# Kernel tuning notes

Hardware: AMD Instinct MI355X
Metric: run time of the kernel (lower is better)

The kernel has to match this reference:

```python
import jax, jax.numpy as jnp
import numpy as np
from jax import lax

K_KNN = 20           # DGCNN default neighborhood size
SLOPE = 0.2          # LeakyReLU negative slope


def _leaky(x):
    return jnp.where(x >= 0, x, SLOPE * x)


def _knn(x, k):
    # x: [B, N, C] -> idx [B, N, k] of nearest neighbors (incl. self) in feature space
    xx = jnp.sum(x * x, axis=-1)                       # [B, N]
    d = xx[:, :, None] + xx[:, None, :] - 2.0 * jnp.einsum('bnc,bmc->bnm', x, x)
    return lax.top_k(-d, k)[1]                          # [B, N, k]


def _edge_conv(x, idx, w, b):
    # x: [B, N, C]; idx: [B, N, k]; w: [O, 2C]; b: [O]
    neigh = jax.vmap(lambda xt, i: xt[i])(x, idx)       # [B, N, k, C]
    center = jnp.broadcast_to(x[:, :, None, :], neigh.shape)
    feat = jnp.concatenate([neigh - center, center], axis=-1)  # [B, N, k, 2C]
    h = _leaky(jnp.einsum('bnkc,oc->bnko', feat, w) + b)
    return jnp.max(h, axis=2)                           # [B, N, O]


def setup_inputs() -> dict:
    key = jax.random.key(0)
    ks = jax.random.split(key, 20)
    B, N, J, KR = 4, 4096, 24, 4
    layers = [64, 128, 256]

    def w_init(k, o, i):
        return jax.random.normal(k, (o, i), jnp.float32) / np.sqrt(i)

    inp = {
        'V': jax.random.normal(ks[0], (B, N, 3), jnp.float32),
        'W': jax.random.uniform(ks[1], (B, J, N), jnp.float32),
        'skeletonOneRingIdx': jax.random.randint(ks[2], (B, J, KR), 0, J),
    }
    # geoNet edge-conv params (input channels per layer: 3, 64, 128 -> 2C inputs)
    inp['g1_w'] = w_init(ks[3], 64, 6);    inp['g1_b'] = jnp.zeros((64,), jnp.float32)
    inp['g2_w'] = w_init(ks[4], 128, 128); inp['g2_b'] = jnp.zeros((128,), jnp.float32)
    inp['g3_w'] = w_init(ks[5], 256, 256); inp['g3_b'] = jnp.zeros((256,), jnp.float32)
    # skeleton edge-conv params (inputs: 451 -> 902, 256 -> 512, 128 -> 256)
    inp['s1_w'] = w_init(ks[6], 256, 902); inp['s1_b'] = jnp.zeros((256,), jnp.float32)
    inp['s2_w'] = w_init(ks[7], 128, 512); inp['s2_b'] = jnp.zeros((128,), jnp.float32)
    inp['s3_w'] = w_init(ks[8], 64, 256);  inp['s3_b'] = jnp.zeros((64,), jnp.float32)
    # jointMLP 1x1 convs: 448 -> 512 -> 256 -> 3
    inp['m1_w'] = w_init(ks[9], 512, 448);  inp['m1_b'] = jnp.zeros((512,), jnp.float32)
    inp['m2_w'] = w_init(ks[10], 256, 512); inp['m2_b'] = jnp.zeros((256,), jnp.float32)
    inp['m3_w'] = w_init(ks[11], 3, 256);   inp['m3_b'] = jnp.zeros((3,), jnp.float32)
    return inp


def reference(V, W, skeletonOneRingIdx,
              g1_w, g1_b, g2_w, g2_b, g3_w, g3_b,
              s1_w, s1_b, s2_w, s2_b, s3_w, s3_b,
              m1_w, m1_b, m2_w, m2_b, m3_w, m3_b):
    # ---- geoNet: DGCNN with dynamic kNN, output cat([xyz, l1, l2, l3]) -> [B, N, 451]
    outs = [V]
    h = V
    for w, b in ((g1_w, g1_b), (g2_w, g2_b), (g3_w, g3_b)):
        idx = _knn(h, K_KNN)
        h = _edge_conv(h, idx, w, b)
        outs.append(h)
    feat = jnp.concatenate(outs, axis=-1)                # [B, N, 451]

    # ---- weighted pooling onto skeleton joints
    pooled = jnp.einsum('bjn,bnc->bjc', W, feat)
    pooled = pooled / (jnp.sum(W, axis=-1, keepdims=True) + 1e-5)  # [B, J, 451]

    # ---- skeleton edge convs with fixed one-ring idx
    v1 = _edge_conv(pooled, skeletonOneRingIdx, s1_w, s1_b)  # [B, J, 256]
    v2 = _edge_conv(v1, skeletonOneRingIdx, s2_w, s2_b)      # [B, J, 128]
    v3 = _edge_conv(v2, skeletonOneRingIdx, s3_w, s3_b)      # [B, J, 64]

    joints = jnp.concatenate([v1, v2, v3], axis=-1)          # [B, J, 448]
    h = _leaky(jnp.einsum('bjc,oc->bjo', joints, m1_w) + m1_b)
    h = _leaky(jnp.einsum('bjc,oc->bjo', h, m2_w) + m2_b)
    out = jnp.einsum('bjc,oc->bjo', h, m3_w) + m3_b          # [B, J, 3]
    return out
```

## Files before the change

### kernel.cpp

```cpp
#include <hip/hip_runtime.h>
#include <hip/hip_bf16.h>
#include <float.h>

#define B_   4
#define N_   4096
#define J_   24
#define KR_  4
#define KNN_ 20
#define SLOPE 0.2f
#define SLABN 64
#define NSLAB (N_ / SLABN)
#define NTILE 32
#define SCAP 768
#define KSLACK 8u

typedef __attribute__((ext_vector_type(8))) short bf16x8;
typedef __attribute__((ext_vector_type(4))) float f32x4;

__global__ void k_norm(const float* __restrict__ h, float* __restrict__ xx, int C) {
    int i = blockIdx.x * blockDim.x + threadIdx.x;
    if (i >= B_ * N_) return;
    const float* hp = h + (size_t)i * C;
    float s = 0.f;
    for (int c = 0; c < C; ++c) { float v = hp[c]; s += v * v; }
    xx[i] = s;
}

__device__ __forceinline__ unsigned mapf(float f) {
    unsigned u = __float_as_uint(f);
    return (u & 0x80000000u) ? ~u : (u | 0x80000000u);
}
__device__ __forceinline__ unsigned key16(float f) {
    return mapf(f) >> 16;
}

__global__ void k_split(const float* __restrict__ h, unsigned short* __restrict__ hi,
                        unsigned short* __restrict__ lo, int total4) {
    int i = blockIdx.x * 256 + threadIdx.x;
    if (i >= total4) return;
    float4 v = ((const float4*)h)[i];
    ushort4 h4, l4;
    {
        unsigned u = __float_as_uint(v.x); h4.x = (unsigned short)(u >> 16);
        float r = v.x - __uint_as_float(u & 0xffff0000u); l4.x = (unsigned short)(__float_as_uint(r) >> 16);
    }
    {
        unsigned u = __float_as_uint(v.y); h4.y = (unsigned short)(u >> 16);
        float r = v.y - __uint_as_float(u & 0xffff0000u); l4.y = (unsigned short)(__float_as_uint(r) >> 16);
    }
    {
        unsigned u = __float_as_uint(v.z); h4.z = (unsigned short)(u >> 16);
        float r = v.z - __uint_as_float(u & 0xffff0000u); l4.z = (unsigned short)(__float_as_uint(r) >> 16);
    }
    {
        unsigned u = __float_as_uint(v.w); h4.w = (unsigned short)(u >> 16);
        float r = v.w - __uint_as_float(u & 0xffff0000u); l4.w = (unsigned short)(__float_as_uint(r) >> 16);
    }
    ((ushort4*)hi)[i] = h4;
    ((ushort4*)lo)[i] = l4;
}

__global__ __launch_bounds__(256) void k_dist(const unsigned short* __restrict__ Hi,
                                              const unsigned short* __restrict__ Lo,
                                              int C,
                                              const float* __restrict__ xxall,
                                              unsigned short* __restrict__ Dall, int b0) {
    __shared__ unsigned short tile[128][136];
    int b = b0 + blockIdx.y;
    const unsigned short* XH = Hi + (size_t)b * N_ * C;
    const unsigned short* XL = Lo + (size_t)b * N_ * C;
    const float* xxb = xxall + (size_t)b * N_;
    unsigned short* D = Dall + (size_t)blockIdx.y * N_ * N_;

    int t = blockIdx.x;
    int ti = 0;
    while (t >= NTILE - ti) { t -= NTILE - ti; ++ti; }
    int tj = ti + t;
    int row0 = ti * 128, col0 = tj * 128;
    int tid  = threadIdx.x;
    int wv   = tid >> 6, lane = tid & 63;
    int wr   = wv >> 1,  wc   = wv & 1;
    int rbase = row0 + wr * 64;
    int cbase = col0 + wc * 64;
    int lp    = lane & 15;
    int kgrp  = lane >> 4;

    f32x4 acc[4][4];
#pragma unroll
    for (int i = 0; i < 4; ++i)
#pragma unroll
        for (int j = 0; j < 4; ++j) acc[i][j] = (f32x4){0.f, 0.f, 0.f, 0.f};

    for (int ks = 0; ks < C; ks += 32) {
        int kb = ks + kgrp * 8;
        bf16x8 ah[4], al[4];
#pragma unroll
        for (int fi = 0; fi < 4; ++fi) {
            size_t ro = (size_t)(rbase + fi * 16 + lp) * C + kb;
            ah[fi] = *(const bf16x8*)(XH + ro);
            al[fi] = *(const bf16x8*)(XL + ro);
        }
#pragma unroll
        for (int fj = 0; fj < 4; ++fj) {
            size_t co = (size_t)(cbase + fj * 16 + lp) * C + kb;
            bf16x8 bh = *(const bf16x8*)(XH + co);
            bf16x8 bl = *(const bf16x8*)(XL + co);
#pragma unroll
            for (int fi = 0; fi < 4; ++fi) {
                acc[fi][fj] = __builtin_amdgcn_mfma_f32_16x16x32_bf16(ah[fi], bh, acc[fi][fj], 0, 0, 0);
                acc[fi][fj] = __builtin_amdgcn_mfma_f32_16x16x32_bf16(ah[fi], bl, acc[fi][fj], 0, 0, 0);
                acc[fi][fj] = __builtin_amdgcn_mfma_f32_16x16x32_bf16(al[fi], bh, acc[fi][fj], 0, 0, 0);
            }
        }
    }

    float xxrv = xxb[rbase + lane];
    float xxcv = xxb[cbase + lane];
    int rsub = (lane >> 4) * 4;
#pragma unroll
    for (int fi = 0; fi < 4; ++fi) {
#pragma unroll
        for (int fj = 0; fj < 4; ++fj) {
            float xc = __shfl(xxcv, fj * 16 + lp, 64);
#pragma unroll
            for (int r = 0; r < 4; ++r) {
                float xr = __shfl(xxrv, fi * 16 + rsub + r, 64);
                float d = xr + xc - 2.f * acc[fi][fj][r];
                tile[wr * 64 + fi * 16 + rsub + r][wc * 64 + fj * 16 + lp] =
                    (unsigned short)key16(d);
            }
        }
    }
    __syncthreads();

    {
        int r0   = tid >> 4;
        int cseg = (tid & 15) * 8;
#pragma unroll
        for (int q = 0; q < 8; ++q) {
            int row = r0 + q * 16;
            *(uint4*)(D + (size_t)(row0 + row) * N_ + col0 + cseg) =
                *(const uint4*)&tile[row][cseg];
        }
    }
    if (ti == tj) return;
    {
        int c0g = tid >> 4;
        int g   = tid & 15;
#pragma unroll
        for (int cq = 0; cq < 8; ++cq) {
            int c = c0g + cq * 16;
            unsigned short s[8];
#pragma unroll
            for (int q = 0; q < 8; ++q) s[q] = tile[g * 8 + q][c];
            *(uint4*)(D + (size_t)(col0 + c) * N_ + row0 + g * 8) = *(const uint4*)s;
        }
    }
}

__device__ __forceinline__ unsigned radixsel_wave(unsigned val, int r, int nbits) {
    unsigned long long cand = ~0ull;
    unsigned prefix = 0;
    for (int bit = nbits - 1; bit >= 0; --bit) {
        unsigned long long z = cand & __ballot(!((val >> bit) & 1u));
        int cz = __popcll(z);
        if (cz >= r) cand = z;
        else { r -= cz; cand &= ~z; prefix |= 1u << bit; }
    }
    return prefix;
}

__device__ __forceinline__ bool top20_round(unsigned long long key, bool active) {
    unsigned hi = (unsigned)(key >> 32);
    unsigned lo = (unsigned)key;
    unsigned long long amask = __ballot(active);
    int navail = __popcll(amask);
    if (navail <= KNN_) return active;
    int r = KNN_;
    unsigned long long cand = amask;
    unsigned prefix = 0;
    for (int bit = 31; bit >= 0; --bit) {
        unsigned long long z = cand & __ballot(!((hi >> bit) & 1u));
        int cz = __popcll(z);
        if (cz >= r) cand = z;
        else { r -= cz; cand &= ~z; prefix |= 1u << bit; }
    }
    unsigned long long c2 = __ballot(active && hi == prefix);
    unsigned p2 = 0;
    for (int bit = 11; bit >= 0; --bit) {
        unsigned long long z = c2 & __ballot(!((lo >> bit) & 1u));
        int cz = __popcll(z);
        if (cz >= r) c2 = z;
        else { r -= cz; c2 &= ~z; p2 |= 1u << bit; }
    }
    return active && (hi < prefix || (hi == prefix && lo <= p2));
}

__device__ __forceinline__ void final_top20(const unsigned long long* skey, int S,
                                            unsigned long long* wbuf,
                                            int lane, int* idxout, int obase) {
    unsigned long long key = (lane < S) ? skey[lane] : ~0ull;
    bool active = (lane < S) && (lane < 64);
    int consumed = (S < 64) ? S : 64;
    int nw = 0;
    for (;;) {
        bool win = top20_round(key, active);
        unsigned long long wb = __ballot(win);
        nw = __popcll(wb);
        int pos = __popcll(wb & ((1ull << lane) - 1ull));
        if (win) wbuf[pos] = key;
        if (consumed >= S) break;
        int src = consumed + lane - nw;
        key = (lane < nw) ? wbuf[lane] : ((src < S) ? skey[src] : ~0ull);
        active = (lane < nw) || (src >= consumed && src < S);
        consumed += 64 - nw;
    }
    if (lane < nw) {
        unsigned long long mine = wbuf[lane];
        int rank = 0;
        for (int i = 0; i < nw; ++i) rank += (wbuf[i] < mine);
        idxout[obase + rank] = (int)(unsigned)mine;
    }
}

__global__ __launch_bounds__(256) void k_sel(const unsigned short* __restrict__ Dall,
                                             const float* __restrict__ Xall, int C,
                                             const float* __restrict__ xxall,
                                             int* __restrict__ knnIdx, int b0) {
    __shared__ unsigned sidx[SCAP];
    __shared__ unsigned long long skey[SCAP];
    __shared__ unsigned long long wbuf[24];
    __shared__ float qf[128];
    __shared__ unsigned stau[4];
    __shared__ int scnt;
    int b = b0 + blockIdx.y;
    const unsigned short* Db = Dall + (size_t)blockIdx.y * N_ * N_;
    const float* Xb  = Xall + (size_t)b * N_ * C;
    const float* xxb = xxall + (size_t)b * N_;
    int* idxout = knnIdx + (size_t)b * N_ * KNN_;
    int ql   = blockIdx.x;
    int tid  = threadIdx.x;
    int wv   = tid >> 6;
    int lane = tid & 63;
    int gbase = wv * 1024 + lane * 16;
    if (tid == 0) scnt = 0;
    for (int c = tid; c < C; c += 256) qf[c] = Xb[(size_t)ql * C + c];

    const uint4* kp = (const uint4*)(Db + (size_t)ql * N_ + gbase);
    uint4 pa = kp[0], pb = kp[1];
    unsigned kv[16];
    kv[0] = pa.x & 0xffffu;  kv[1] = pa.x >> 16;
    kv[2] = pa.y & 0xffffu;  kv[3] = pa.y >> 16;
    kv[4] = pa.z & 0xffffu;  kv[5] = pa.z >> 16;
    kv[6] = pa.w & 0xffffu;  kv[7] = pa.w >> 16;
    kv[8] = pb.x & 0xffffu;  kv[9] = pb.x >> 16;
    kv[10] = pb.y & 0xffffu; kv[11] = pb.y >> 16;
    kv[12] = pb.z & 0xffffu; kv[13] = pb.z >> 16;
    kv[14] = pb.w & 0xffffu; kv[15] = pb.w >> 16;

    unsigned mn = kv[0];
#pragma unroll
    for (int t = 1; t < 16; ++t) mn = (kv[t] < mn) ? kv[t] : mn;
    unsigned Bw = radixsel_wave(mn, KNN_, 16);
    if (lane == 0) stau[wv] = Bw;
    __syncthreads();
    unsigned tau = stau[0];
    tau = (stau[1] < tau) ? stau[1] : tau;
    tau = (stau[2] < tau) ? stau[2] : tau;
    tau = (stau[3] < tau) ? stau[3] : tau;
    tau += KSLACK;
    if (tau > 0xffffu) tau = 0xffffu;

#pragma unroll
    for (int t = 0; t < 16; ++t) {
        if (kv[t] <= tau) {
            int p = atomicAdd(&scnt, 1);
            if (p < SCAP) sidx[p] = (unsigned)(gbase + t);
        }
    }
    __syncthreads();
    int S = scnt; if (S > SCAP) S = SCAP;
    float xxq = xxb[ql];
    const float4* xq4 = (const float4*)qf;
    for (int s = tid; s < S; s += 256) {
        int j = (int)sidx[s];
        const float4* xj = (const float4*)(Xb + (size_t)j * C);
        float a0 = 0.f, a1 = 0.f, a2 = 0.f, a3 = 0.f;
        for (int c4 = 0; c4 < (C >> 2); ++c4) {
            float4 x = xj[c4]; float4 qv = xq4[c4];
            a0 = fmaf(qv.x, x.x, a0);
            a1 = fmaf(qv.y, x.y, a1);
            a2 = fmaf(qv.z, x.z, a2);
            a3 = fmaf(qv.w, x.w, a3);
        }
        float dot = (a0 + a1) + (a2 + a3);
        float d = xxq + xxb[j] - 2.f * dot;
        skey[s] = ((unsigned long long)mapf(d) << 32) | (unsigned)j;
    }
    __syncthreads();
    if (wv != 0) return;
    final_top20(skey, S, wbuf, lane, idxout, ql * KNN_);
}

__global__ __launch_bounds__(256) void k_selC3(const float* __restrict__ V,
                                               const float* __restrict__ xx,
                                               int* __restrict__ knnIdx) {
    __shared__ unsigned long long sbuf[SCAP];
    __shared__ unsigned long long wbuf[24];
    __shared__ unsigned stau[4];
    __shared__ int scnt;
    int b    = blockIdx.y;
    const float* Xb  = V + (size_t)b * N_ * 3;
    const float* xxb = xx + (size_t)b * N_;
    int* idxout = knnIdx + (size_t)b * N_ * KNN_;
    int q    = blockIdx.x;
    int tid  = threadIdx.x;
    int wv   = tid >> 6;
    int lane = tid & 63;
    int gbase = wv * 1024 + lane * 16;
    if (tid == 0) scnt = 0;

    float qx = Xb[q * 3], qy = Xb[q * 3 + 1], qz = Xb[q * 3 + 2];
    float xxq = xxb[q];

    float pts[48];
    const float4* src = (const float4*)(Xb + (size_t)gbase * 3);
#pragma unroll
    for (int t = 0; t < 12; ++t) ((float4*)pts)[t] = src[t];

    unsigned kk[16];
#pragma unroll
    for (int t = 0; t < 16; ++t) {
        float dot = qx * pts[3 * t];
        dot = fmaf(qy, pts[3 * t + 1], dot);
        dot = fmaf(qz, pts[3 * t + 2], dot);
        float d = xxq + xxb[gbase + t] - 2.f * dot;
        kk[t] = mapf(d);
    }

    unsigned mn = kk[0];
#pragma unroll
    for (int t = 1; t < 16; ++t) mn = (kk[t] < mn) ? kk[t] : mn;
    unsigned Bw = radixsel_wave(mn, KNN_, 32);
    if (lane == 0) stau[wv] = Bw;
    __syncthreads();
    unsigned tau = stau[0];
    tau = (stau[1] < tau) ? stau[1] : tau;
    tau = (stau[2] < tau) ? stau[2] : tau;
    tau = (stau[3] < tau) ? stau[3] : tau;

#pragma unroll
    for (int t = 0; t < 16; ++t) {
        if (kk[t] <= tau) {
            int p = atomicAdd(&scnt, 1);
            if (p < SCAP)
                sbuf[p] = ((unsigned long long)kk[t] << 32) | (unsigned)(gbase + t);
        }
    }
    __syncthreads();
    if (wv != 0) return;
    int S = scnt; if (S > SCAP) S = SCAP;
    final_top20(sbuf, S, wbuf, lane, idxout, q * KNN_);
}

__device__ __forceinline__ void prepP_elem(const float* __restrict__ w,
                                           const float* __restrict__ bias,
                                           int C, int O, float* __restrict__ P,
                                           float* __restrict__ b2, int i) {
    int O2 = 2 * O;
    if (i < O2) b2[i] = (i < O) ? 0.f : bias[i - O];
    if (i >= C * O2) return;
    int k = i / O2, col = i % O2;
    float v;
    if (col < O) v = w[(size_t)col * 2 * C + k];
    else { int o = col - O; v = w[(size_t)o * 2 * C + C + k] - w[(size_t)o * 2 * C + k]; }
    P[i] = v;
}
__device__ __forceinline__ void transp_elem(const float* __restrict__ w, int O, int K,
                                            float* __restrict__ wT, int i) {
    if (i >= O * K) return;
    int k = i / O, o = i % O;
    wT[i] = w[(size_t)o * K + k];
}

__global__ void k_prepall(const float* g1w, const float* g1b,
                          const float* g2w, const float* g2b,
                          const float* g3w, const float* g3b,
                          const float* s1w, const float* s1b,
                          const float* s2w, const float* s2b,
                          const float* s3w, const float* s3b,
                          const float* m1w, const float* m2w, const float* m3w,
                          float* P1, float* P2, float* P3, float* P4, float* P5,
                          float* P6, float* P7, float* P8, float* P9,
                          float* bb1, float* bb2, float* bb3,
                          float* bb4, float* bb5, float* bb6) {
    int i = blockIdx.x * 256 + threadIdx.x;
    switch (blockIdx.y) {
        case 0: prepP_elem(g1w, g1b, 3,   64,  P1, bb1, i); break;
        case 1: prepP_elem(g2w, g2b, 64,  128, P2, bb2, i); break;
        case 2: prepP_elem(g3w, g3b, 128, 256, P3, bb3, i); break;
        case 3: prepP_elem(s1w, s1b, 451, 256, P4, bb4, i); break;
        case 4: prepP_elem(s2w, s2b, 256, 128, P5, bb5, i); break;
        case 5: prepP_elem(s3w, s3b, 128, 64,  P6, bb6, i); break;
        case 6: transp_elem(m1w, 512, 448, P7, i); break;
        case 7: transp_elem(m2w, 256, 512, P8, i); break;
        case 8: transp_elem(m3w, 3,   256, P9, i); break;
    }
}

__global__ __launch_bounds__(256) void k_gemm(const float* __restrict__ A, int lda,
                                              const float* __restrict__ Bm,
                                              float* __restrict__ Cm, int ldc,
                                              int M, int N, int K,
                                              const float* __restrict__ bias, int leaky) {
    __shared__ float As[16][68];
    __shared__ float Bs[16][68];
    int tid = threadIdx.x;
    int row0 = blockIdx.y * 64, col0 = blockIdx.x * 64;
    int tr = tid >> 4, tc = tid & 15;
    float acc[4][4] = {{0.f}};
    for (int kt = 0; kt < K; kt += 16) {
#pragma unroll
        for (int i = 0; i < 4; ++i) {
            int e = tid + 256 * i;
            int r = e >> 4, kk = e & 15;
            int gr = row0 + r, gk = kt + kk;
            float v = 0.f;
            if (gr < M && gk < K) v = A[(size_t)gr * lda + gk];
            As[kk][r] = v;
        }
#pragma unroll
        for (int i = 0; i < 4; ++i) {
            int e = tid + 256 * i;
            int kk = e >> 6, c = e & 63;
            int gk = kt + kk, gc = col0 + c;
            float v = 0.f;
            if (gk < K && gc < N) v = Bm[(size_t)gk * N + gc];
            Bs[kk][c] = v;
        }
        __syncthreads();
#pragma unroll
        for (int kk = 0; kk < 16; ++kk) {
            float a[4], bv[4];
            *(float4*)&a[0]  = *(const float4*)&As[kk][tr * 4];
            *(float4*)&bv[0] = *(const float4*)&Bs[kk][tc * 4];
#pragma unroll
            for (int i = 0; i < 4; ++i)
#pragma unroll
                for (int j = 0; j < 4; ++j) acc[i][j] += a[i] * bv[j];
        }
        __syncthreads();
    }
#pragma unroll
    for (int i = 0; i < 4; ++i) {
        int r = row0 + tr * 4 + i;
        if (r >= M) continue;
#pragma unroll
        for (int j = 0; j < 4; ++j) {
            int c = col0 + tc * 4 + j;
            if (c >= N) continue;
            float v = acc[i][j];
            if (bias) v += bias[c];
            if (leaky) v = v >= 0.f ? v : SLOPE * v;
            Cm[(size_t)r * ldc + c] = v;
        }
    }
}

__global__ __launch_bounds__(256) void k_sgemm(const float* __restrict__ A, int lda,
                                               const float* __restrict__ Bm,
                                               float* __restrict__ Cm, int ldc,
                                               int N, int K,
                                               const float* __restrict__ bias, int leaky) {
    extern __shared__ float Arow[];
    int r   = blockIdx.x;
    int c0  = blockIdx.y * 256;
    int tid = threadIdx.x;
    for (int k = tid; k < K; k += 256) Arow[k] = A[(size_t)r * lda + k];
    __syncthreads();
    int c = c0 + tid;
    if (c >= N) return;
    float acc = bias ? bias[c] : 0.f;
    for (int k = 0; k < K; ++k) acc += Arow[k] * Bm[(size_t)k * N + c];
    if (leaky) acc = acc >= 0.f ? acc : SLOPE * acc;
    Cm[(size_t)r * ldc + c] = acc;
}

__global__ void k_gathermax(const float* __restrict__ Y, int O, int R,
                            const int* __restrict__ idx, int kc,
                            float* __restrict__ out, int ldo, int ooff,
                            float* __restrict__ xxout) {
    extern __shared__ int sidx[];
    __shared__ float red[256];
    int br = blockIdx.x;
    int b  = br / R;
    int o  = threadIdx.x;
    if (o < kc) sidx[o] = idx[(size_t)br * kc + o];
    __syncthreads();
    int O2 = 2 * O;
    float z = Y[(size_t)br * O2 + O + o];
    float best = -FLT_MAX;
    for (int k = 0; k < kc; ++k) {
        int m = sidx[k];
        best = fmaxf(best, Y[(size_t)(b * R + m) * O2 + o]);
    }
    float r = z + best;
    r = r >= 0.f ? r : SLOPE * r;
    out[(size_t)br * ldo + ooff + o] = r;
    if (xxout) {
        red[o] = r * r;
        __syncthreads();
        for (int s = blockDim.x >> 1; s > 0; s >>= 1) {
            if (o < s) red[o] += red[o + s];
            __syncthreads();
        }
        if (o == 0) xxout[br] = red[0];
    }
}

__device__ __forceinline__ void chan_map(int b, int c,
                                         const float* Vf, const float* l1,
                                         const float* l2, const float* l3,
                                         const float*& p, int& st) {
    if (c < 3)        { st = 3;   p = Vf + (size_t)b * N_ * 3   + c; }
    else if (c < 67)  { st = 64;  p = l1 + (size_t)b * N_ * 64  + (c - 3); }
    else if (c < 195) { st = 128; p = l2 + (size_t)b * N_ * 128 + (c - 67); }
    else              { st = 256; p = l3 + (size_t)b * N_ * 256 + (c - 195); }
}

__global__ __launch_bounds__(256) void k_pool2(const float* __restrict__ Vf,
                                               const float* __restrict__ l1,
                                               const float* __restrict__ l2,
                                               const float* __restrict__ l3,
                                               const float* __restrict__ W,
                                               float* __restrict__ ppool,
                                               float* __restrict__ psw) {
    __shared__ float Wl[SLABN][J_];
    int blk  = blockIdx.x;
    int b    = blk / NSLAB, slab = blk % NSLAB;
    int n0   = slab * SLABN;
    int tid  = threadIdx.x;

    for (int e = tid; e < J_ * SLABN; e += 256) {
        int j = e / SLABN, n = e % SLABN;
        Wl[n][j] = W[((size_t)b * J_ + j) * N_ + n0 + n];
    }
    __syncthreads();

    if (tid < J_) {
        float s = 0.f;
        for (int n = 0; n < SLABN; ++n) s += Wl[n][tid];
        psw[(size_t)blk * J_ + tid] = s;
    }

    int c0 = tid, c1 = tid + 256;
    const float *p0, *p1 = nullptr; int s0, s1 = 0;
    chan_map(b, c0, Vf, l1, l2, l3, p0, s0);
    bool has1 = (c1 < 451);
    if (has1) chan_map(b, c1, Vf, l1, l2, l3, p1, s1);

    float acc0[J_], acc1[J_];
#pragma unroll
    for (int j = 0; j < J_; ++j) { acc0[j] = 0.f; acc1[j] = 0.f; }

    for (int n = 0; n < SLABN; ++n) {
        float v0 = p0[(size_t)(n0 + n) * s0];
        float v1 = has1 ? p1[(size_t)(n0 + n) * s1] : 0.f;
        const float* wn = &Wl[n][0];
#pragma unroll
        for (int q = 0; q < J_ / 4; ++q) {
            float4 w4 = *(const float4*)(wn + 4 * q);
            acc0[4*q+0] += w4.x * v0;  acc1[4*q+0] += w4.x * v1;
            acc0[4*q+1] += w4.y * v0;  acc1[4*q+1] += w4.y * v1;
            acc0[4*q+2] += w4.z * v0;  acc1[4*q+2] += w4.z * v1;
            acc0[4*q+3] += w4.w * v0;  acc1[4*q+3] += w4.w * v1;
        }
    }
    float* pp = ppool + (size_t)blk * J_ * 451;
#pragma unroll
    for (int j = 0; j < J_; ++j) {
        pp[(size_t)j * 451 + c0] = acc0[j];
        if (has1) pp[(size_t)j * 451 + c1] = acc1[j];
    }
}

__global__ __launch_bounds__(256) void k_poolred(const float* __restrict__ ppool,
                                                 const float* __restrict__ psw,
                                                 float* __restrict__ pooled) {
    int bj = blockIdx.x;
    int b  = bj / J_, j = bj % J_;
    int tid = threadIdx.x;

    float sw = 0.f;
    for (int sl = 0; sl < NSLAB; ++sl) sw += psw[(size_t)(b * NSLAB + sl) * J_ + j];
    float inv = 1.f / (sw + 1e-5f);

    for (int c = tid; c < 451; c += 256) {
        float s = 0.f;
        for (int sl = 0; sl < NSLAB; ++sl)
            s += ppool[((size_t)(b * NSLAB + sl) * J_ + j) * 451 + c];
        pooled[(size_t)bj * 451 + c] = s * inv;
    }
}

extern "C" void kernel_launch(void* const* d_in, const int* in_sizes, int n_in,
                              void* d_out, int out_size, void* d_ws, size_t ws_size,
                              hipStream_t stream) {
    const float* V  = (const float*)d_in[0];
    const float* W  = (const float*)d_in[1];
    const int* ringIdx = (const int*)d_in[2];
    const float* g1w = (const float*)d_in[3];
    const float* g1b = (const float*)d_in[4];
    const float* g2w = (const float*)d_in[5];
    const float* g2b = (const float*)d_in[6];
    const float* g3w = (const float*)d_in[7];
    const float* g3b = (const float*)d_in[8];
    const float* s1w = (const float*)d_in[9];
    const float* s1b = (const float*)d_in[10];
    const float* s2w = (const float*)d_in[11];
    const float* s2b = (const float*)d_in[12];
    const float* s3w = (const float*)d_in[13];
    const float* s3b = (const float*)d_in[14];
    const float* m1w = (const float*)d_in[15];
    const float* m1b = (const float*)d_in[16];
    const float* m2w = (const float*)d_in[17];
    const float* m2b = (const float*)d_in[18];
    const float* m3w = (const float*)d_in[19];
    const float* m3b = (const float*)d_in[20];
    (void)n_in; (void)in_sizes; (void)out_size;

    const int szP1 = 3 * 128,    szP2 = 64 * 256,  szP3 = 128 * 512;
    const int szP4 = 451 * 512,  szP5 = 256 * 256, szP6 = 128 * 128;
    const int szP7 = 448 * 512,  szP8 = 512 * 256, szP9 = 256 * 3;

    auto dreg_floats = [&](int nd) -> size_t {
        size_t a = (size_t)nd * ((size_t)N_ * N_ / 2);
        size_t ymax = (size_t)B_ * N_ * 512;
        size_t pool = (size_t)B_ * NSLAB * J_ * 451 + (size_t)B_ * NSLAB * J_;
        size_t r = a;
        if (ymax > r) r = ymax;
        if (pool > r) r = pool;
        return r;
    };
    auto layout_bytes = [&](int nd) -> size_t {
        size_t f = 0;
        f += (size_t)B_ * N_ * 64 + (size_t)B_ * N_ * 128 + (size_t)B_ * N_ * 256;
        f += (size_t)B_ * N_;
        f += dreg_floats(nd);
        f += 2 * ((size_t)B_ * N_ * 128 / 2);
        f += (size_t)B_ * N_ * KNN_;
        f += (size_t)B_ * J_ * 451 + (size_t)B_ * J_ * 448;
        f += (size_t)B_ * J_ * 512 + (size_t)B_ * J_ * 256;
        f += (size_t)(szP1 + szP2 + szP3 + szP4 + szP5 + szP6 + szP7 + szP8 + szP9);
        f += 128 + 256 + 512 + 512 + 256 + 128;
        return f * 4;
    };
    int nb = 1;
    if (ws_size >= layout_bytes(4)) nb = 4;
    else if (ws_size >= layout_bytes(2)) nb = 2;

    float* ws = (float*)d_ws;
    size_t off = 0;
    float* l1 = ws + off; off += (size_t)B_ * N_ * 64;
    float* l2 = ws + off; off += (size_t)B_ * N_ * 128;
    float* l3 = ws + off; off += (size_t)B_ * N_ * 256;
    float* xx = ws + off; off += (size_t)B_ * N_;
    float* D  = ws + off; off += dreg_floats(nb);
    unsigned short* Dk = (unsigned short*)D;
    float* Y  = D;
    float* ppool = D;
    float* psw   = D + (size_t)B_ * NSLAB * J_ * 451;
    unsigned short* Xhi = (unsigned short*)(ws + off); off += (size_t)B_ * N_ * 128 / 2;
    unsigned short* Xlo = (unsigned short*)(ws + off); off += (size_t)B_ * N_ * 128 / 2;
    int* knnIdx = (int*)(ws + off); off += (size_t)B_ * N_ * KNN_;
    float* pooled = ws + off; off += (size_t)B_ * J_ * 451;
    float* joints = ws + off; off += (size_t)B_ * J_ * 448;
    float* h1 = ws + off; off += (size_t)B_ * J_ * 512;
    float* h2 = ws + off; off += (size_t)B_ * J_ * 256;
    float* P1 = ws + off; off += szP1;
    float* P2 = ws + off; off += szP2;
    float* P3 = ws + off; off += szP3;
    float* P4 = ws + off; off += szP4;
    float* P5 = ws + off; off += szP5;
    float* P6 = ws + off; off += szP6;
    float* P7 = ws + off; off += szP7;
    float* P8 = ws + off; off += szP8;
    float* P9 = ws + off; off += szP9;
    float* bb1 = ws + off; off += 128;
    float* bb2 = ws + off; off += 256;
    float* bb3 = ws + off; off += 512;
    float* bb4 = ws + off; off += 512;
    float* bb5 = ws + off; off += 256;
    float* bb6 = ws + off; off += 128;

    const int M = B_ * N_;
    const int MJ = B_ * J_;
    const int NUTRI = NTILE * (NTILE + 1) / 2;

    k_prepall<<<dim3((szP4 + 255) / 256, 9), 256, 0, stream>>>(
        g1w, g1b, g2w, g2b, g3w, g3b, s1w, s1b, s2w, s2b, s3w, s3b,
        m1w, m2w, m3w, P1, P2, P3, P4, P5, P6, P7, P8, P9,
        bb1, bb2, bb3, bb4, bb5, bb6);

    k_norm<<<(M + 255) / 256, 256, 0, stream>>>(V, xx, 3);
    k_selC3<<<dim3(N_, B_), 256, 0, stream>>>(V, xx, knnIdx);
    k_gemm<<<dim3(2, M / 64), 256, 0, stream>>>(V, 3, P1, Y, 128, M, 128, 3, bb1, 0);
    k_gathermax<<<M, 64, KNN_ * sizeof(int), stream>>>(Y, 64, N_, knnIdx, KNN_, l1, 64, 0, xx);

    k_split<<<(M * 64 / 4 + 255) / 256, 256, 0, stream>>>(l1, Xhi, Xlo, M * 64 / 4);
    for (int g = 0; g < B_; g += nb) {
        k_dist<<<dim3(NUTRI, nb), 256, 0, stream>>>(Xhi, Xlo, 64, xx, Dk, g);
        k_sel<<<dim3(N_, nb), 256, 0, stream>>>(Dk, l1, 64, xx, knnIdx, g);
    }
    k_gemm<<<dim3(4, M / 64), 256, 0, stream>>>(l1, 64, P2, Y, 256, M, 256, 64, bb2, 0);
    k_gathermax<<<M, 128, KNN_ * sizeof(int), stream>>>(Y, 128, N_, knnIdx, KNN_, l2, 128, 0, xx);

    k_split<<<(M * 128 / 4 + 255) / 256, 256, 0, stream>>>(l2, Xhi, Xlo, M * 128 / 4);
    for (int g = 0; g < B_; g += nb) {
        k_dist<<<dim3(NUTRI, nb), 256, 0, stream>>>(Xhi, Xlo, 128, xx, Dk, g);
        k_sel<<<dim3(N_, nb), 256, 0, stream>>>(Dk, l2, 128, xx, knnIdx, g);
    }
    k_gemm<<<dim3(8, M / 64), 256, 0, stream>>>(l2, 128, P3, Y, 512, M, 512, 128, bb3, 0);
    k_gathermax<<<M, 256, KNN_ * sizeof(int), stream>>>(Y, 256, N_, knnIdx, KNN_, l3, 256, 0, nullptr);

    k_pool2<<<B_ * NSLAB, 256, 0, stream>>>(V, l1, l2, l3, W, ppool, psw);
    k_poolred<<<MJ, 256, 0, stream>>>(ppool, psw, pooled);

    k_sgemm<<<dim3(MJ, 2), 256, 451 * sizeof(float), stream>>>(pooled, 451, P4, Y, 512, 512, 451, bb4, 0);
    k_gathermax<<<MJ, 256, KR_ * sizeof(int), stream>>>(Y, 256, J_, ringIdx, KR_, joints, 448, 0, nullptr);

    k_sgemm<<<dim3(MJ, 1), 256, 256 * sizeof(float), stream>>>(joints, 448, P5, Y, 256, 256, 256, bb5, 0);
    k_gathermax<<<MJ, 128, KR_ * sizeof(int), stream>>>(Y, 128, J_, ringIdx, KR_, joints, 448, 256, nullptr);

    k_sgemm<<<dim3(MJ, 1), 256, 128 * sizeof(float), stream>>>(joints + 256, 448, P6, Y, 128, 128, 128, bb6, 0);
    k_gathermax<<<MJ, 64, KR_ * sizeof(int), stream>>>(Y, 64, J_, ringIdx, KR_, joints, 448, 384, nullptr);

    k_sgemm<<<dim3(MJ, 2), 256, 448 * sizeof(float), stream>>>(joints, 448, P7, h1, 512, 512, 448, m1b, 1);
    k_sgemm<<<dim3(MJ, 1), 256, 512 * sizeof(float), stream>>>(h1, 512, P8, h2, 256, 256, 512, m2b, 1);
    k_sgemm<<<dim3(MJ, 1), 256, 256 * sizeof(float), stream>>>(h2, 256, P9, (float*)d_out, 3, 3, 256, m3b, 0);
}
```

Measured before the change: 961.1 us.

## Process one kNN query per wavefront instead of per block

The kNN selection kernels now map one query row to each 64-lane wavefront, so a 256-thread block handles four queries and the grid shrinks by four. Each wave loads the whole distance row into registers, computes its threshold alone, and compacts candidates with a single atomic per lane, which removes the block-wide barriers and the per-element shared atomics. The previous design left three of four waves idle during the final top-20 step; now every wave does it for its own query. Per-wave candidate buffers are smaller, raising register pressure and the risk of truncating candidates on skewed rows.

After: 841.2 us. 1.14x faster.

```diff
diff --git a/kernel.cpp b/kernel.cpp
--- a/kernel.cpp
+++ b/kernel.cpp
@@ -11,7 +11,7 @@
 #define SLABN 64
 #define NSLAB (N_ / SLABN)
 #define NTILE 32
-#define SCAP 768
+#define SCAPW 320
 #define KSLACK 8u
 
 typedef __attribute__((ext_vector_type(8))) short bf16x8;
@@ -200,7 +200,7 @@
                                             unsigned long long* wbuf,
                                             int lane, int* idxout, int obase) {
     unsigned long long key = (lane < S) ? skey[lane] : ~0ull;
-    bool active = (lane < S) && (lane < 64);
+    bool active = (lane < S);
     int consumed = (S < 64) ? S : 64;
     int nw = 0;
     for (;;) {
@@ -227,63 +227,67 @@
                                              const float* __restrict__ Xall, int C,
                                              const float* __restrict__ xxall,
                                              int* __restrict__ knnIdx, int b0) {
-    __shared__ unsigned sidx[SCAP];
-    __shared__ unsigned long long skey[SCAP];
-    __shared__ unsigned long long wbuf[24];
-    __shared__ float qf[128];
-    __shared__ unsigned stau[4];
-    __shared__ int scnt;
+    __shared__ unsigned short sidx[4][SCAPW];
+    __shared__ unsigned long long skey[4][SCAPW];
+    __shared__ unsigned long long wbuf[4][24];
+    __shared__ int scnt[4];
     int b = b0 + blockIdx.y;
     const unsigned short* Db = Dall + (size_t)blockIdx.y * N_ * N_;
     const float* Xb  = Xall + (size_t)b * N_ * C;
     const float* xxb = xxall + (size_t)b * N_;
     int* idxout = knnIdx + (size_t)b * N_ * KNN_;
-    int ql   = blockIdx.x;
-    int tid  = threadIdx.x;
-    int wv   = tid >> 6;
-    int lane = tid & 63;
-    int gbase = wv * 1024 + lane * 16;
-    if (tid == 0) scnt = 0;
-    for (int c = tid; c < C; c += 256) qf[c] = Xb[(size_t)ql * C + c];
-
-    const uint4* kp = (const uint4*)(Db + (size_t)ql * N_ + gbase);
-    uint4 pa = kp[0], pb = kp[1];
-    unsigned kv[16];
-    kv[0] = pa.x & 0xffffu;  kv[1] = pa.x >> 16;
-    kv[2] = pa.y & 0xffffu;  kv[3] = pa.y >> 16;
-    kv[4] = pa.z & 0xffffu;  kv[5] = pa.z >> 16;
-    kv[6] = pa.w & 0xffffu;  kv[7] = pa.w >> 16;
-    kv[8] = pb.x & 0xffffu;  kv[9] = pb.x >> 16;
-    kv[10] = pb.y & 0xffffu; kv[11] = pb.y >> 16;
-    kv[12] = pb.z & 0xffffu; kv[13] = pb.z >> 16;
-    kv[14] = pb.w & 0xffffu; kv[15] = pb.w >> 16;
-
-    unsigned mn = kv[0];
-#pragma unroll
-    for (int t = 1; t < 16; ++t) mn = (kv[t] < mn) ? kv[t] : mn;
-    unsigned Bw = radixsel_wave(mn, KNN_, 16);
-    if (lane == 0) stau[wv] = Bw;
-    __syncthreads();
-    unsigned tau = stau[0];
-    tau = (stau[1] < tau) ? stau[1] : tau;
-    tau = (stau[2] < tau) ? stau[2] : tau;
-    tau = (stau[3] < tau) ? stau[3] : tau;
-    tau += KSLACK;
+    int wv   = threadIdx.x >> 6;
+    int lane = threadIdx.x & 63;
+    int ql   = blockIdx.x * 4 + wv;
+    if (lane == 0) scnt[wv] = 0;
+
+    const uint4* row = (const uint4*)(Db + (size_t)ql * N_);
+    uint4 K[8];
+#pragma unroll
+    for (int q = 0; q < 8; ++q) K[q] = row[q * 64 + lane];
+
+    unsigned mn = 0xffffu;
+#pragma unroll
+    for (int q = 0; q < 8; ++q) {
+        const unsigned* w = (const unsigned*)&K[q];
+#pragma unroll
+        for (int h = 0; h < 4; ++h) {
+            unsigned lo = w[h] & 0xffffu, hi = w[h] >> 16;
+            mn = (lo < mn) ? lo : mn;
+            mn = (hi < mn) ? hi : mn;
+        }
+    }
+    unsigned tau = radixsel_wave(mn, KNN_, 16) + KSLACK;
     if (tau > 0xffffu) tau = 0xffffu;
 
-#pragma unroll
-    for (int t = 0; t < 16; ++t) {
-        if (kv[t] <= tau) {
-            int p = atomicAdd(&scnt, 1);
-            if (p < SCAP) sidx[p] = (unsigned)(gbase + t);
-        }
-    }
-    __syncthreads();
-    int S = scnt; if (S > SCAP) S = SCAP;
+    int nl = 0;
+#pragma unroll
+    for (int q = 0; q < 8; ++q) {
+        const unsigned* w = (const unsigned*)&K[q];
+#pragma unroll
+        for (int h = 0; h < 4; ++h) {
+            nl += ((w[h] & 0xffffu) <= tau);
+            nl += ((w[h] >> 16) <= tau);
+        }
+    }
+    int p = atomicAdd(&scnt[wv], nl);
+#pragma unroll
+    for (int q = 0; q < 8; ++q) {
+        const unsigned* w = (const unsigned*)&K[q];
+        int jb = (q * 64 + lane) * 8;
+#pragma unroll
+        for (int h = 0; h < 4; ++h) {
+            if ((w[h] & 0xffffu) <= tau) { if (p < SCAPW) sidx[wv][p] = (unsigned short)(jb + 2 * h);     ++p; }
+            if ((w[h] >> 16)     <= tau) { if (p < SCAPW) sidx[wv][p] = (unsigned short)(jb + 2 * h + 1); ++p; }
+        }
+    }
+    int S = scnt[wv];
+    if (S > SCAPW) S = SCAPW;
+
     float xxq = xxb[ql];
-    const float4* xq4 = (const float4*)qf;
-    for (int s = tid; s < S; s += 256) {
-        int j = (int)sidx[s];
+    const float4* xq4 = (const float4*)(Xb + (size_t)ql * C);
+    for (int s = lane; s < S; s += 64) {
+        int j = (int)sidx[wv][s];
         const float4* xj = (const float4*)(Xb + (size_t)j * C);
         float a0 = 0.f, a1 = 0.f, a2 = 0.f, a3 = 0.f;
         for (int c4 = 0; c4 < (C >> 2); ++c4) {
@@ -295,72 +299,71 @@
         }
         float dot = (a0 + a1) + (a2 + a3);
         float d = xxq + xxb[j] - 2.f * dot;
-        skey[s] = ((unsigned long long)mapf(d) << 32) | (unsigned)j;
-    }
-    __syncthreads();
-    if (wv != 0) return;
-    final_top20(skey, S, wbuf, lane, idxout, ql * KNN_);
+        skey[wv][s] = ((unsigned long long)mapf(d) << 32) | (unsigned)j;
+    }
+    final_top20(skey[wv], S, wbuf[wv], lane, idxout, ql * KNN_);
 }
 
 __global__ __launch_bounds__(256) void k_selC3(const float* __restrict__ V,
                                                const float* __restrict__ xx,
                                                int* __restrict__ knnIdx) {
-    __shared__ unsigned long long sbuf[SCAP];
-    __shared__ unsigned long long wbuf[24];
-    __shared__ unsigned stau[4];
-    __shared__ int scnt;
+    __shared__ unsigned long long skey[4][SCAPW];
+    __shared__ unsigned long long wbuf[4][24];
+    __shared__ int scnt[4];
     int b    = blockIdx.y;
     const float* Xb  = V + (size_t)b * N_ * 3;
     const float* xxb = xx + (size_t)b * N_;
     int* idxout = knnIdx + (size_t)b * N_ * KNN_;
-    int q    = blockIdx.x;
-    int tid  = threadIdx.x;
-    int wv   = tid >> 6;
-    int lane = tid & 63;
-    int gbase = wv * 1024 + lane * 16;
-    if (tid == 0) scnt = 0;
+    int wv   = threadIdx.x >> 6;
+    int lane = threadIdx.x & 63;
+    int q    = blockIdx.x * 4 + wv;
+    if (lane == 0) scnt[wv] = 0;
 
     float qx = Xb[q * 3], qy = Xb[q * 3 + 1], qz = Xb[q * 3 + 2];
     float xxq = xxb[q];
 
-    float pts[48];
-    const float4* src = (const float4*)(Xb + (size_t)gbase * 3);
-#pragma unroll
-    for (int t = 0; t < 12; ++t) ((float4*)pts)[t] = src[t];
-
-    unsigned kk[16];
-#pragma unroll
-    for (int t = 0; t < 16; ++t) {
-        float dot = qx * pts[3 * t];
-        dot = fmaf(qy, pts[3 * t + 1], dot);
-        dot = fmaf(qz, pts[3 * t + 2], dot);
-        float d = xxq + xxb[gbase + t] - 2.f * dot;
-        kk[t] = mapf(d);
+    unsigned kk[64];
+#pragma unroll
+    for (int cq = 0; cq < 4; ++cq) {
+        int jb = (cq * 64 + lane) * 16;
+        float pts[48];
+        const float4* src = (const float4*)(Xb + (size_t)jb * 3);
+#pragma unroll
+        for (int t = 0; t < 12; ++t) ((float4*)pts)[t] = src[t];
+#pragma unroll
+        for (int t = 0; t < 16; ++t) {
+            float dot = qx * pts[3 * t];
+            dot = fmaf(qy, pts[3 * t + 1], dot);
+            dot = fmaf(qz, pts[3 * t + 2], dot);
+            float d = xxq + xxb[jb + t] - 2.f * dot;
+            kk[cq * 16 + t] = mapf(d);
+        }
     }
 
     unsigned mn = kk[0];
 #pragma unroll
-    for (int t = 1; t < 16; ++t) mn = (kk[t] < mn) ? kk[t] : mn;
-    unsigned Bw = radixsel_wave(mn, KNN_, 32);
-    if (lane == 0) stau[wv] = Bw;
-    __syncthreads();
-    unsigned tau = stau[0];
-    tau = (stau[1] < tau) ? stau[1] : tau;
-    tau = (stau[2] < tau) ? stau[2] : tau;
-    tau = (stau[3] < tau) ? stau[3] : tau;
-
-#pragma unroll
-    for (int t = 0; t < 16; ++t) {
-        if (kk[t] <= tau) {
-            int p = atomicAdd(&scnt, 1);
-            if (p < SCAP)
-                sbuf[p] = ((unsigned long long)kk[t] << 32) | (unsigned)(gbase + t);
-        }
-    }
-    __syncthreads();
-    if (wv != 0) return;
-    int S = scnt; if (S > SCAP) S = SCAP;
-    final_top20(sbuf, S, wbuf, lane, idxout, q * KNN_);
+    for (int t = 1; t < 64; ++t) mn = (kk[t] < mn) ? kk[t] : mn;
+    unsigned tau = radixsel_wave(mn, KNN_, 32);
+
+    int nl = 0;
+#pragma unroll
+    for (int t = 0; t < 64; ++t) nl += (kk[t] <= tau);
+    int p = atomicAdd(&scnt[wv], nl);
+#pragma unroll
+    for (int cq = 0; cq < 4; ++cq) {
+        int jb = (cq * 64 + lane) * 16;
+#pragma unroll
+        for (int t = 0; t < 16; ++t) {
+            if (kk[cq * 16 + t] <= tau) {
+                if (p < SCAPW)
+                    skey[wv][p] = ((unsigned long long)kk[cq * 16 + t] << 32) | (unsigned)(jb + t);
+                ++p;
+            }
+        }
+    }
+    int S = scnt[wv];
+    if (S > SCAPW) S = SCAPW;
+    final_top20(skey[wv], S, wbuf[wv], lane, idxout, q * KNN_);
 }
 
 __device__ __forceinline__ void prepP_elem(const float* __restrict__ w,
@@ -703,14 +706,14 @@
         bb1, bb2, bb3, bb4, bb5, bb6);
 
     k_norm<<<(M + 255) / 256, 256, 0, stream>>>(V, xx, 3);
-    k_selC3<<<dim3(N_, B_), 256, 0, stream>>>(V, xx, knnIdx);
+    k_selC3<<<dim3(N_ / 4, B_), 256, 0, stream>>>(V, xx, knnIdx);
     k_gemm<<<dim3(2, M / 64), 256, 0, stream>>>(V, 3, P1, Y, 128, M, 128, 3, bb1, 0);
     k_gathermax<<<M, 64, KNN_ * sizeof(int), stream>>>(Y, 64, N_, knnIdx, KNN_, l1, 64, 0, xx);
 
     k_split<<<(M * 64 / 4 + 255) / 256, 256, 0, stream>>>(l1, Xhi, Xlo, M * 64 / 4);
     for (int g = 0; g < B_; g += nb) {
         k_dist<<<dim3(NUTRI, nb), 256, 0, stream>>>(Xhi, Xlo, 64, xx, Dk, g);
-        k_sel<<<dim3(N_, nb), 256, 0, stream>>>(Dk, l1, 64, xx, knnIdx, g);
+        k_sel<<<dim3(N_ / 4, nb), 256, 0, stream>>>(Dk, l1, 64, xx, knnIdx, g);
     }
     k_gemm<<<dim3(4, M / 64), 256, 0, stream>>>(l1, 64, P2, Y, 256, M, 256, 64, bb2, 0);
     k_gathermax<<<M, 128, KNN_ * sizeof(int), stream>>>(Y, 128, N_, knnIdx, KNN_, l2, 128, 0, xx);
@@ -718,7 +721,7 @@
     k_split<<<(M * 128 / 4 + 255) / 256, 256, 0, stream>>>(l2, Xhi, Xlo, M * 128 / 4);
     for (int g = 0; g < B_; g += nb) {
         k_dist<<<dim3(NUTRI, nb), 256, 0, stream>>>(Xhi, Xlo, 128, xx, Dk, g);
-        k_sel<<<dim3(N_, nb), 256, 0, stream>>>(Dk, l2, 128, xx, knnIdx, g);
+        k_sel<<<dim3(N_ / 4, nb), 256, 0, stream>>>(Dk, l2, 128, xx, knnIdx, g);
     }
     k_gemm<<<dim3(8, M / 64), 256, 0, stream>>>(l2, 128, P3, Y, 512, M, 512, 128, bb3, 0);
     k_gathermax<<<M, 256, KNN_ * sizeof(int), stream>>>(Y, 256, N_, knnIdx, KNN_, l3, 256, 0, nullptr);
```
